# Performance work log

Hardware: AMD Instinct MI355X
Metric: run time of the kernel (lower is better)

Reference implementation:

```python
import jax, jax.numpy as jnp
import numpy as np

D_MODEL = 1024
NHEAD = 16
HEAD_DIM = D_MODEL // NHEAD


def setup_inputs() -> dict:
    key = jax.random.key(0)
    ks = jax.random.split(key, 7)
    N, S, E = 2, 2048, D_MODEL
    query = jax.random.normal(ks[0], (N, S, E), dtype=jnp.float32)
    key_t = jax.random.normal(ks[1], (N, S, E), dtype=jnp.float32)
    value = jax.random.normal(ks[2], (N, S, E), dtype=jnp.float32)
    # nn.Linear default init scale ~ 1/sqrt(fan_in)
    s = 1.0 / np.sqrt(E)
    w_in = jax.random.uniform(ks[3], (3 * E, E), jnp.float32, -s, s)
    b_in = jax.random.uniform(ks[4], (3 * E,), jnp.float32, -s, s)
    w_o = jax.random.uniform(ks[5], (E, E), jnp.float32, -s, s)
    b_o = jax.random.uniform(ks[6], (E,), jnp.float32, -s, s)
    return {"query": query, "key": key_t, "value": value,
            "w_in": w_in, "b_in": b_in, "w_o": w_o, "b_o": b_o}


def reference(query, key, value, w_in, b_in, w_o, b_o):
    # NOTE: the torch module computes q,k,v all from `query` (self-attention);
    # the `key`/`value` args are ignored by its forward math.
    N, S, E = query.shape
    H, Dh = NHEAD, HEAD_DIM
    qkv = query @ w_in.T + b_in                      # (N, S, 3E)
    q, k, v = jnp.split(qkv, 3, axis=-1)
    def heads(x):
        return x.reshape(N, S, H, Dh).transpose(0, 2, 1, 3)  # (N, H, S, Dh)
    q, k, v = heads(q), heads(k), heads(v)
    scale = 1.0 / jnp.sqrt(jnp.asarray(Dh, query.dtype))
    scores = jnp.einsum('bhqd,bhkd->bhqk', q, k) * scale     # (N, H, S, S)
    attn = jax.nn.softmax(scores, axis=-1)
    out = jnp.einsum('bhqk,bhkd->bhqd', attn, v)             # (N, H, S, Dh)
    out = out.transpose(0, 2, 1, 3).reshape(N, S, E)
    return out @ w_o.T + b_o
```

## Files before the change

### kernel.cpp

```cpp
#include <hip/hip_runtime.h>
#include <hip/hip_bf16.h>
#include <stdint.h>

#define NB   2
#define SEQ  2048
#define EMB  1024
#define NH   16
#define DH   64
#define MR   (NB*SEQ)
#define E3   (3*EMB)
#define CSC  (0.125f * 1.44269504f)

typedef __attribute__((ext_vector_type(8))) short bf16x8;
typedef __attribute__((ext_vector_type(4))) float f32x4;
typedef __attribute__((ext_vector_type(16))) float f32x16;

__device__ __forceinline__ unsigned short f2bf(float f) {
  unsigned u = __float_as_uint(f);
  unsigned r = (u + 0x7FFF + ((u >> 16) & 1)) >> 16;
  return (unsigned short)r;
}
__device__ __forceinline__ unsigned pack2(float lo, float hi) {
  return (unsigned)f2bf(lo) | ((unsigned)f2bf(hi) << 16);
}
__device__ __forceinline__ float bf2f(unsigned short s) {
  return __uint_as_float(((unsigned)s) << 16);
}
__device__ __forceinline__ unsigned cvtpk(float lo, float hi) {
  unsigned r;
  asm("v_cvt_pk_bf16_f32 %0, %1, %2" : "=v"(r) : "v"(lo), "v"(hi));
  return r;
}

__device__ __forceinline__ void gld16(const unsigned short* g, unsigned short* l) {
  __builtin_amdgcn_global_load_lds(
      (const __attribute__((address_space(1))) unsigned int*)g,
      (__attribute__((address_space(3))) unsigned int*)l,
      16, 0, 0);
}

__global__ void cvt_all(const float* __restrict__ q,
                        const float* __restrict__ w_in,
                        const float* __restrict__ w_o,
                        unsigned short* __restrict__ Xbf,
                        unsigned short* __restrict__ Winbf,
                        unsigned short* __restrict__ Wobf) {
  int b = blockIdx.x;
  const float* src; unsigned short* dst; int off;
  if (b < 2048)      { src = q;    dst = Xbf;   off = b; }
  else if (b < 3584) { src = w_in; dst = Winbf; off = b - 2048; }
  else               { src = w_o;  dst = Wobf;  off = b - 3584; }
  int i = (off * 256 + threadIdx.x) * 8;
  float4 a = *(const float4*)(src + i);
  float4 c = *(const float4*)(src + i + 4);
  uint4 o;
  o.x = pack2(a.x, a.y);
  o.y = pack2(a.z, a.w);
  o.z = pack2(c.x, c.y);
  o.w = pack2(c.z, c.w);
  *(uint4*)(dst + i) = o;
}

template<int BN, bool OUT_F32>
__global__ __launch_bounds__(256) void gemm_bt(
    const unsigned short* __restrict__ A,
    const unsigned short* __restrict__ Bt,
    const float* __restrict__ bias,
    void* __restrict__ Cout,
    int K, int ldc, int scale_cols) {
  constexpr int NR = BN / 32;
  constexpr int WNT = BN / 2;
  __shared__ unsigned short As[4096];
  __shared__ unsigned short Bs[BN * 32];
  const int tid  = threadIdx.x;
  const int lane = tid & 63;
  const int w    = tid >> 6;
  const int wm = w >> 1, wn = w & 1;
  const int g = lane >> 4, li = lane & 15;
  const int rowBase = blockIdx.x * 128;
  const int colBase = blockIdx.y * BN;

  f32x4 acc[4][NR];
#pragma unroll
  for (int m = 0; m < 4; ++m)
#pragma unroll
    for (int nn = 0; nn < NR; ++nn) { acc[m][nn][0]=0.f; acc[m][nn][1]=0.f; acc[m][nn][2]=0.f; acc[m][nn][3]=0.f; }

  const unsigned short* Ag = A  + (size_t)(rowBase + (tid >> 2)) * K + (tid & 3) * 8;
  const unsigned short* Bg = Bt + (size_t)(colBase + (tid >> 2)) * K + (tid & 3) * 8;

  for (int k0 = 0; k0 < K; k0 += 32) {
    __syncthreads();
    gld16(Ag + k0,                As + tid * 8);
    gld16(Ag + (size_t)64*K + k0, As + 2048 + tid * 8);
    gld16(Bg + k0,                Bs + tid * 8);
    if (BN == 128)
      gld16(Bg + (size_t)64*K + k0, Bs + 2048 + tid * 8);
    __syncthreads();

    bf16x8 af[4], bfv[NR];
#pragma unroll
    for (int m = 0; m < 4; ++m)
      af[m] = *(const bf16x8*)&As[(wm*64 + m*16 + li) * 32 + g * 8];
#pragma unroll
    for (int nn = 0; nn < NR; ++nn)
      bfv[nn] = *(const bf16x8*)&Bs[(wn*WNT + nn*16 + li) * 32 + g * 8];
#pragma unroll
    for (int m = 0; m < 4; ++m)
#pragma unroll
      for (int nn = 0; nn < NR; ++nn)
        acc[m][nn] = __builtin_amdgcn_mfma_f32_16x16x32_bf16(af[m], bfv[nn], acc[m][nn], 0, 0, 0);
  }

#pragma unroll
  for (int nn = 0; nn < NR; ++nn) {
    const int col = colBase + wn*WNT + nn*16 + li;
    const float bv = bias[col];
    const float sc = (col < scale_cols) ? CSC : 1.0f;
#pragma unroll
    for (int m = 0; m < 4; ++m) {
      const int r0 = rowBase + wm*64 + m*16 + g*4;
#pragma unroll
      for (int r = 0; r < 4; ++r) {
        float v = (acc[m][nn][r] + bv) * sc;
        if (OUT_F32) ((float*)Cout)[(size_t)(r0 + r) * ldc + col] = v;
        else ((unsigned short*)Cout)[(size_t)(r0 + r) * ldc + col] = f2bf(v);
      }
    }
  }
}

__global__ __launch_bounds__(256, 3) void attn32(
    const unsigned short* __restrict__ qkv,
    unsigned short* __restrict__ x2) {
  __shared__ unsigned short smem[16384];
  char* LB = (char*)smem;

  const int tid  = threadIdx.x;
  const int lane = tid & 63;
  const int w    = tid >> 6;
  const int hi   = lane >> 5;
  const int l31  = lane & 31;
  const int slot = blockIdx.x;
  const int bid  = (slot & 7) * 64 + (slot >> 3);
  const int qb = bid & 15, h = (bid >> 4) & 15, n = bid >> 8;
  const size_t rowN = (size_t)n * SEQ;
  const int vp_ = tid & 31, dblk = tid >> 5;
  const int vps = (vp_ & ~6) | ((vp_ & 2) << 1) | ((vp_ & 4) >> 1);

  bf16x8 qf[4];
  {
    const size_t qr = rowN + qb*128 + w*32 + l31;
#pragma unroll
    for (int kc = 0; kc < 4; ++kc)
      qf[kc] = *(const bf16x8*)&qkv[qr * E3 + h*64 + kc*16 + hi*8];
  }

  f32x16 ZEROV;
#pragma unroll
  for (int i = 0; i < 16; ++i) ZEROV[i] = 0.f;
  f32x16 acc0 = ZEROV, acc1 = ZEROV;
  float ssum[8];
#pragma unroll
  for (int i = 0; i < 8; ++i) ssum[i] = 0.f;

  uint4 pv0, pv1;
  auto stageK = [&](int kt, int buf) {
#pragma unroll
    for (int p = 0; p < 2; ++p) {
      int r = p*32 + (tid >> 3);
      int ch = (tid & 7) ^ (r & 7);
      gld16(&qkv[(rowN + kt + r) * E3 + EMB + h*64 + ch*8],
            &smem[buf*4096 + p*2048 + tid*8]);
    }
  };
  auto loadV = [&](int kt) {
    const unsigned short* vp = &qkv[(rowN + kt + 2*vp_) * E3 + 2*EMB + h*64 + dblk*8];
    pv0 = *(const uint4*)vp;
    pv1 = *(const uint4*)(vp + E3);
  };
  auto writeV = [&](int buf) {
    const unsigned short* s0 = (const unsigned short*)&pv0;
    const unsigned short* s1 = (const unsigned short*)&pv1;
#pragma unroll
    for (int j = 0; j < 8; ++j) {
      int d = dblk*8 + j;
      unsigned val = (unsigned)s0[j] | ((unsigned)s1[j] << 16);
      *(unsigned*)(LB + 16384 + buf*8192 + d*128 + (((vps>>2) ^ (d&7)) << 4) + (vps&3)*4) = val;
    }
  };

  loadV(0);
  stageK(0, 0);
  writeV(0);
  __syncthreads();

  for (int t = 0; t < 32; ++t) {
    const int cur = t & 1;
    const bool pre = (t + 1 < 32);
    const int ktn = (t + 1) * 64;
    if (pre) { loadV(ktn); stageK(ktn, cur^1); }

    const char* Kb = LB + cur*8192;
    bf16x8 ka[4], kb[4];
#pragma unroll
    for (int kc = 0; kc < 4; ++kc) {
      const int sw = ((kc*2 + hi) ^ (l31 & 7)) << 4;
      ka[kc] = *(const bf16x8*)(Kb + l31*128 + sw);
      kb[kc] = *(const bf16x8*)(Kb + 4096 + l31*128 + sw);
    }
    __builtin_amdgcn_s_setprio(1);
    f32x16 z0 = __builtin_amdgcn_mfma_f32_32x32x16_bf16(ka[0], qf[0], ZEROV, 0, 0, 0);
    f32x16 z1 = __builtin_amdgcn_mfma_f32_32x32x16_bf16(kb[0], qf[0], ZEROV, 0, 0, 0);
#pragma unroll
    for (int kc = 1; kc < 4; ++kc) {
      z0 = __builtin_amdgcn_mfma_f32_32x32x16_bf16(ka[kc], qf[kc], z0, 0, 0, 0);
      z1 = __builtin_amdgcn_mfma_f32_32x32x16_bf16(kb[kc], qf[kc], z1, 0, 0, 0);
    }
    __builtin_amdgcn_s_setprio(0);

#pragma unroll
    for (int i = 0; i < 16; ++i) {
      z0[i] = __builtin_amdgcn_exp2f(z0[i]);
      z1[i] = __builtin_amdgcn_exp2f(z1[i]);
    }
#pragma unroll
    for (int i = 0; i < 8; ++i)
      ssum[i] += (z0[2*i] + z0[2*i+1]) + (z1[2*i] + z1[2*i+1]);

    bf16x8 pf[4];
    {
      union { bf16x8 v; unsigned u[4]; } r0_, r1_, r2_, r3_;
#pragma unroll
      for (int j = 0; j < 4; ++j) {
        r0_.u[j] = cvtpk(z0[2*j],     z0[2*j + 1]);
        r1_.u[j] = cvtpk(z0[8 + 2*j], z0[9 + 2*j]);
        r2_.u[j] = cvtpk(z1[2*j],     z1[2*j + 1]);
        r3_.u[j] = cvtpk(z1[8 + 2*j], z1[9 + 2*j]);
      }
      pf[0] = r0_.v; pf[1] = r1_.v; pf[2] = r2_.v; pf[3] = r3_.v;
    }

    if (pre) writeV(cur ^ 1);

    const char* Vb = LB + 16384 + cur*8192;
    __builtin_amdgcn_s_setprio(1);
#pragma unroll
    for (int c = 0; c < 4; ++c) {
      const int sw = ((c*2 + hi) ^ (l31 & 7)) << 4;
      bf16x8 va = *(const bf16x8*)(Vb + l31*128 + sw);
      bf16x8 vb = *(const bf16x8*)(Vb + 4096 + l31*128 + sw);
      acc0 = __builtin_amdgcn_mfma_f32_32x32x16_bf16(va, pf[c], acc0, 0, 0, 0);
      acc1 = __builtin_amdgcn_mfma_f32_32x32x16_bf16(vb, pf[c], acc1, 0, 0, 0);
    }
    __builtin_amdgcn_s_setprio(0);
    __syncthreads();
  }

#pragma unroll
  for (int st = 4; st; st >>= 1)
#pragma unroll
    for (int i = 0; i < st; ++i) ssum[i] += ssum[i + st];
  float lsum = ssum[0] + __shfl_xor(ssum[0], 32);

  float rn = 1.0f / lsum;
  const int qrow_l = w*32 + l31;
#pragma unroll
  for (int dt = 0; dt < 2; ++dt) {
#pragma unroll
    for (int r = 0; r < 16; r += 2) {
      float v0 = (dt ? acc1[r]   : acc0[r])   * rn;
      float v1 = (dt ? acc1[r+1] : acc0[r+1]) * rn;
      int d = dt*32 + (r & 3) + 8*(r >> 2) + 4*hi;
      unsigned val = pack2(v0, v1);
      int col32 = d >> 1;
      int g = col32 >> 2;
      *(unsigned*)(LB + qrow_l*128 + ((g ^ (qrow_l & 7)) << 4) + (col32 & 3)*4) = val;
    }
  }
  __syncthreads();
  {
    int row = tid >> 1;
    size_t orow = (rowN + qb*128 + row) * EMB + h*64;
#pragma unroll
    for (int i = 0; i < 4; ++i) {
      int gg = (tid & 1)*4 + i;
      uint4 v = *(const uint4*)(LB + row*128 + ((gg ^ (row & 7)) << 4));
      *(uint4*)&x2[orow + gg*8] = v;
    }
  }
}

extern "C" void kernel_launch(void* const* d_in, const int* in_sizes, int n_in,
                              void* d_out, int out_size, void* d_ws, size_t ws_size,
                              hipStream_t stream) {
  const float* q    = (const float*)d_in[0];
  const float* w_in = (const float*)d_in[3];
  const float* b_in = (const float*)d_in[4];
  const float* w_o  = (const float*)d_in[5];
  const float* b_o  = (const float*)d_in[6];

  char* ws = (char*)d_ws;
  unsigned short* Wobf  = (unsigned short*)(ws);
  unsigned short* Xbf   = (unsigned short*)(ws + 2097152);
  unsigned short* Winbf = (unsigned short*)(ws + 10485760);
  unsigned short* QKV   = (unsigned short*)(ws + 16777216);
  unsigned short* X2    = (unsigned short*)(ws + 41943040);

  cvt_all<<<4096, 256, 0, stream>>>(q, w_in, w_o, Xbf, Winbf, Wobf);

  gemm_bt<128, false><<<dim3(32, 24), 256, 0, stream>>>(Xbf, Winbf, b_in, (void*)QKV, EMB, E3, 1024);
  attn32<<<NB * NH * (SEQ / 128), 256, 0, stream>>>(QKV, X2);
  gemm_bt<64, true><<<dim3(32, 16), 256, 0, stream>>>(X2, Wobf, b_o, d_out, EMB, EMB, 0);
}
```

Measured before the change: 117.0 us.

## Process two 64-key tiles per barrier in attention loop

Each main-loop iteration of the attention kernel now stages and consumes 128 keys (two 64-row K/V sub-tiles) instead of 64. That halves the number of __syncthreads barriers and prefetch rounds. Shared memory doubles to 64KB and launch bounds drop from 3 to 2 blocks per CU, trading occupancy for fewer synchronisations and larger prefetch batches. More V data is held in registers during prefetch, which raises register pressure.

Result: no change. 117.4 us (+0.3%).

```diff
diff --git a/kernel.cpp b/kernel.cpp
--- a/kernel.cpp
+++ b/kernel.cpp
@@ -130,10 +130,10 @@
   }
 }
 
-__global__ __launch_bounds__(256, 3) void attn32(
+__global__ __launch_bounds__(256, 2) void attn32(
     const unsigned short* __restrict__ qkv,
     unsigned short* __restrict__ x2) {
-  __shared__ unsigned short smem[16384];
+  __shared__ unsigned short smem[32768];
   char* LB = (char*)smem;
 
   const int tid  = threadIdx.x;
@@ -164,96 +164,111 @@
 #pragma unroll
   for (int i = 0; i < 8; ++i) ssum[i] = 0.f;
 
-  uint4 pv0, pv1;
-  auto stageK = [&](int kt, int buf) {
+  uint4 pvA0, pvA1, pvB0, pvB1;
+
+  auto stageK = [&](int kt, int base) {
 #pragma unroll
     for (int p = 0; p < 2; ++p) {
       int r = p*32 + (tid >> 3);
       int ch = (tid & 7) ^ (r & 7);
       gld16(&qkv[(rowN + kt + r) * E3 + EMB + h*64 + ch*8],
-            &smem[buf*4096 + p*2048 + tid*8]);
+            &smem[base + p*2048 + tid*8]);
     }
   };
-  auto loadV = [&](int kt) {
+  auto loadV = [&](int kt, uint4& v0, uint4& v1) {
     const unsigned short* vp = &qkv[(rowN + kt + 2*vp_) * E3 + 2*EMB + h*64 + dblk*8];
-    pv0 = *(const uint4*)vp;
-    pv1 = *(const uint4*)(vp + E3);
+    v0 = *(const uint4*)vp;
+    v1 = *(const uint4*)(vp + E3);
   };
-  auto writeV = [&](int buf) {
-    const unsigned short* s0 = (const unsigned short*)&pv0;
-    const unsigned short* s1 = (const unsigned short*)&pv1;
+  auto writeV = [&](int base, const uint4& v0, const uint4& v1) {
+    const unsigned short* s0 = (const unsigned short*)&v0;
+    const unsigned short* s1 = (const unsigned short*)&v1;
 #pragma unroll
     for (int j = 0; j < 8; ++j) {
       int d = dblk*8 + j;
       unsigned val = (unsigned)s0[j] | ((unsigned)s1[j] << 16);
-      *(unsigned*)(LB + 16384 + buf*8192 + d*128 + (((vps>>2) ^ (d&7)) << 4) + (vps&3)*4) = val;
+      *(unsigned*)(LB + base + d*128 + (((vps>>2) ^ (d&7)) << 4) + (vps&3)*4) = val;
     }
   };
 
-  loadV(0);
-  stageK(0, 0);
-  writeV(0);
+  loadV(0,  pvA0, pvA1);
+  loadV(64, pvB0, pvB1);
+  stageK(0,  0);
+  stageK(64, 4096);
+  writeV(32768,        pvA0, pvA1);
+  writeV(32768 + 8192, pvB0, pvB1);
   __syncthreads();
 
-  for (int t = 0; t < 32; ++t) {
+  for (int t = 0; t < 16; ++t) {
     const int cur = t & 1;
-    const bool pre = (t + 1 < 32);
-    const int ktn = (t + 1) * 64;
-    if (pre) { loadV(ktn); stageK(ktn, cur^1); }
-
-    const char* Kb = LB + cur*8192;
-    bf16x8 ka[4], kb[4];
-#pragma unroll
-    for (int kc = 0; kc < 4; ++kc) {
-      const int sw = ((kc*2 + hi) ^ (l31 & 7)) << 4;
-      ka[kc] = *(const bf16x8*)(Kb + l31*128 + sw);
-      kb[kc] = *(const bf16x8*)(Kb + 4096 + l31*128 + sw);
-    }
-    __builtin_amdgcn_s_setprio(1);
-    f32x16 z0 = __builtin_amdgcn_mfma_f32_32x32x16_bf16(ka[0], qf[0], ZEROV, 0, 0, 0);
-    f32x16 z1 = __builtin_amdgcn_mfma_f32_32x32x16_bf16(kb[0], qf[0], ZEROV, 0, 0, 0);
-#pragma unroll
-    for (int kc = 1; kc < 4; ++kc) {
-      z0 = __builtin_amdgcn_mfma_f32_32x32x16_bf16(ka[kc], qf[kc], z0, 0, 0, 0);
-      z1 = __builtin_amdgcn_mfma_f32_32x32x16_bf16(kb[kc], qf[kc], z1, 0, 0, 0);
-    }
-    __builtin_amdgcn_s_setprio(0);
-
-#pragma unroll
-    for (int i = 0; i < 16; ++i) {
-      z0[i] = __builtin_amdgcn_exp2f(z0[i]);
-      z1[i] = __builtin_amdgcn_exp2f(z1[i]);
-    }
-#pragma unroll
-    for (int i = 0; i < 8; ++i)
-      ssum[i] += (z0[2*i] + z0[2*i+1]) + (z1[2*i] + z1[2*i+1]);
-
-    bf16x8 pf[4];
-    {
-      union { bf16x8 v; unsigned u[4]; } r0_, r1_, r2_, r3_;
-#pragma unroll
-      for (int j = 0; j < 4; ++j) {
-        r0_.u[j] = cvtpk(z0[2*j],     z0[2*j + 1]);
-        r1_.u[j] = cvtpk(z0[8 + 2*j], z0[9 + 2*j]);
-        r2_.u[j] = cvtpk(z1[2*j],     z1[2*j + 1]);
-        r3_.u[j] = cvtpk(z1[8 + 2*j], z1[9 + 2*j]);
-      }
-      pf[0] = r0_.v; pf[1] = r1_.v; pf[2] = r2_.v; pf[3] = r3_.v;
-    }
-
-    if (pre) writeV(cur ^ 1);
-
-    const char* Vb = LB + 16384 + cur*8192;
-    __builtin_amdgcn_s_setprio(1);
-#pragma unroll
-    for (int c = 0; c < 4; ++c) {
-      const int sw = ((c*2 + hi) ^ (l31 & 7)) << 4;
-      bf16x8 va = *(const bf16x8*)(Vb + l31*128 + sw);
-      bf16x8 vb = *(const bf16x8*)(Vb + 4096 + l31*128 + sw);
-      acc0 = __builtin_amdgcn_mfma_f32_32x32x16_bf16(va, pf[c], acc0, 0, 0, 0);
-      acc1 = __builtin_amdgcn_mfma_f32_32x32x16_bf16(vb, pf[c], acc1, 0, 0, 0);
-    }
-    __builtin_amdgcn_s_setprio(0);
+    const bool pre = (t + 1 < 16);
+    const int ktn = (t + 1) * 128;
+    if (pre) {
+      loadV(ktn,      pvA0, pvA1);
+      loadV(ktn + 64, pvB0, pvB1);
+      stageK(ktn,      (cur^1)*8192);
+      stageK(ktn + 64, (cur^1)*8192 + 4096);
+    }
+
+#pragma unroll
+    for (int sub = 0; sub < 2; ++sub) {
+      const char* Kb = LB + (cur*2 + sub)*8192;
+      bf16x8 ka[4], kb[4];
+#pragma unroll
+      for (int kc = 0; kc < 4; ++kc) {
+        const int sw = ((kc*2 + hi) ^ (l31 & 7)) << 4;
+        ka[kc] = *(const bf16x8*)(Kb + l31*128 + sw);
+        kb[kc] = *(const bf16x8*)(Kb + 4096 + l31*128 + sw);
+      }
+      __builtin_amdgcn_s_setprio(1);
+      f32x16 z0 = __builtin_amdgcn_mfma_f32_32x32x16_bf16(ka[0], qf[0], ZEROV, 0, 0, 0);
+      f32x16 z1 = __builtin_amdgcn_mfma_f32_32x32x16_bf16(kb[0], qf[0], ZEROV, 0, 0, 0);
+#pragma unroll
+      for (int kc = 1; kc < 4; ++kc) {
+        z0 = __builtin_amdgcn_mfma_f32_32x32x16_bf16(ka[kc], qf[kc], z0, 0, 0, 0);
+        z1 = __builtin_amdgcn_mfma_f32_32x32x16_bf16(kb[kc], qf[kc], z1, 0, 0, 0);
+      }
+      __builtin_amdgcn_s_setprio(0);
+
+#pragma unroll
+      for (int i = 0; i < 16; ++i) {
+        z0[i] = __builtin_amdgcn_exp2f(z0[i]);
+        z1[i] = __builtin_amdgcn_exp2f(z1[i]);
+      }
+#pragma unroll
+      for (int i = 0; i < 8; ++i)
+        ssum[i] += (z0[2*i] + z0[2*i+1]) + (z1[2*i] + z1[2*i+1]);
+
+      bf16x8 pf[4];
+      {
+        union { bf16x8 v; unsigned u[4]; } r0_, r1_, r2_, r3_;
+#pragma unroll
+        for (int j = 0; j < 4; ++j) {
+          r0_.u[j] = cvtpk(z0[2*j],     z0[2*j + 1]);
+          r1_.u[j] = cvtpk(z0[8 + 2*j], z0[9 + 2*j]);
+          r2_.u[j] = cvtpk(z1[2*j],     z1[2*j + 1]);
+          r3_.u[j] = cvtpk(z1[8 + 2*j], z1[9 + 2*j]);
+        }
+        pf[0] = r0_.v; pf[1] = r1_.v; pf[2] = r2_.v; pf[3] = r3_.v;
+      }
+
+      if (sub == 0 && pre) {
+        writeV(32768 + (cur^1)*16384,        pvA0, pvA1);
+        writeV(32768 + (cur^1)*16384 + 8192, pvB0, pvB1);
+      }
+
+      const char* Vb = LB + 32768 + (cur*2 + sub)*8192;
+      __builtin_amdgcn_s_setprio(1);
+#pragma unroll
+      for (int c = 0; c < 4; ++c) {
+        const int sw = ((c*2 + hi) ^ (l31 & 7)) << 4;
+        bf16x8 va = *(const bf16x8*)(Vb + l31*128 + sw);
+        bf16x8 vb = *(const bf16x8*)(Vb + 4096 + l31*128 + sw);
+        acc0 = __builtin_amdgcn_mfma_f32_32x32x16_bf16(va, pf[c], acc0, 0, 0, 0);
+        acc1 = __builtin_amdgcn_mfma_f32_32x32x16_bf16(vb, pf[c], acc1, 0, 0, 0);
+      }
+      __builtin_amdgcn_s_setprio(0);
+    }
     __syncthreads();
   }
 
```

## Process two query subtiles per wave to reuse K/V tiles in attention

Applied to the files above, without the earlier changes.

Each attention block now covers 256 query rows, with every wave computing two 32-row query groups against the same K and V LDS tiles. The aim is to halve K/V global loads and LDS staging per query and to amortise the barriers. In exchange the grid halves to one block per CU, register pressure rises (launch bounds lowered to 1), and there are fewer waves to hide latency.

Result: slower. 124.6 us (+6.5%).

```diff
diff --git a/kernel.cpp b/kernel.cpp
--- a/kernel.cpp
+++ b/kernel.cpp
@@ -130,7 +130,7 @@
   }
 }
 
-__global__ __launch_bounds__(256, 3) void attn32(
+__global__ __launch_bounds__(256, 1) void attn32(
     const unsigned short* __restrict__ qkv,
     unsigned short* __restrict__ x2) {
   __shared__ unsigned short smem[16384];
@@ -142,27 +142,30 @@
   const int hi   = lane >> 5;
   const int l31  = lane & 31;
   const int slot = blockIdx.x;
-  const int bid  = (slot & 7) * 64 + (slot >> 3);
-  const int qb = bid & 15, h = (bid >> 4) & 15, n = bid >> 8;
+  const int bid  = (slot & 7) * 32 + (slot >> 3);
+  const int qb = bid & 7, h = (bid >> 3) & 15, n = bid >> 7;
   const size_t rowN = (size_t)n * SEQ;
   const int vp_ = tid & 31, dblk = tid >> 5;
   const int vps = (vp_ & ~6) | ((vp_ & 2) << 1) | ((vp_ & 4) >> 1);
 
-  bf16x8 qf[4];
+  bf16x8 qf[2][4];
   {
-    const size_t qr = rowN + qb*128 + w*32 + l31;
-#pragma unroll
-    for (int kc = 0; kc < 4; ++kc)
-      qf[kc] = *(const bf16x8*)&qkv[qr * E3 + h*64 + kc*16 + hi*8];
+    const size_t qr0 = rowN + qb*256 + w*64 + l31;
+#pragma unroll
+    for (int g = 0; g < 2; ++g)
+#pragma unroll
+      for (int kc = 0; kc < 4; ++kc)
+        qf[g][kc] = *(const bf16x8*)&qkv[(qr0 + g*32) * E3 + h*64 + kc*16 + hi*8];
   }
 
   f32x16 ZEROV;
 #pragma unroll
   for (int i = 0; i < 16; ++i) ZEROV[i] = 0.f;
-  f32x16 acc0 = ZEROV, acc1 = ZEROV;
-  float ssum[8];
-#pragma unroll
-  for (int i = 0; i < 8; ++i) ssum[i] = 0.f;
+  f32x16 aA0 = ZEROV, aA1 = ZEROV;
+  f32x16 aB0 = ZEROV, aB1 = ZEROV;
+  float sA[8], sB[8];
+#pragma unroll
+  for (int i = 0; i < 8; ++i) { sA[i] = 0.f; sB[i] = 0.f; }
 
   uint4 pv0, pv1;
   auto stageK = [&](int kt, int buf) {
@@ -209,16 +212,16 @@
       ka[kc] = *(const bf16x8*)(Kb + l31*128 + sw);
       kb[kc] = *(const bf16x8*)(Kb + 4096 + l31*128 + sw);
     }
+
     __builtin_amdgcn_s_setprio(1);
-    f32x16 z0 = __builtin_amdgcn_mfma_f32_32x32x16_bf16(ka[0], qf[0], ZEROV, 0, 0, 0);
-    f32x16 z1 = __builtin_amdgcn_mfma_f32_32x32x16_bf16(kb[0], qf[0], ZEROV, 0, 0, 0);
+    f32x16 z0 = __builtin_amdgcn_mfma_f32_32x32x16_bf16(ka[0], qf[0][0], ZEROV, 0, 0, 0);
+    f32x16 z1 = __builtin_amdgcn_mfma_f32_32x32x16_bf16(kb[0], qf[0][0], ZEROV, 0, 0, 0);
 #pragma unroll
     for (int kc = 1; kc < 4; ++kc) {
-      z0 = __builtin_amdgcn_mfma_f32_32x32x16_bf16(ka[kc], qf[kc], z0, 0, 0, 0);
-      z1 = __builtin_amdgcn_mfma_f32_32x32x16_bf16(kb[kc], qf[kc], z1, 0, 0, 0);
+      z0 = __builtin_amdgcn_mfma_f32_32x32x16_bf16(ka[kc], qf[0][kc], z0, 0, 0, 0);
+      z1 = __builtin_amdgcn_mfma_f32_32x32x16_bf16(kb[kc], qf[0][kc], z1, 0, 0, 0);
     }
     __builtin_amdgcn_s_setprio(0);
-
 #pragma unroll
     for (int i = 0; i < 16; ++i) {
       z0[i] = __builtin_amdgcn_exp2f(z0[i]);
@@ -226,9 +229,8 @@
     }
 #pragma unroll
     for (int i = 0; i < 8; ++i)
-      ssum[i] += (z0[2*i] + z0[2*i+1]) + (z1[2*i] + z1[2*i+1]);
-
-    bf16x8 pf[4];
+      sA[i] += (z0[2*i] + z0[2*i+1]) + (z1[2*i] + z1[2*i+1]);
+    bf16x8 pf0[4];
     {
       union { bf16x8 v; unsigned u[4]; } r0_, r1_, r2_, r3_;
 #pragma unroll
@@ -238,20 +240,61 @@
         r2_.u[j] = cvtpk(z1[2*j],     z1[2*j + 1]);
         r3_.u[j] = cvtpk(z1[8 + 2*j], z1[9 + 2*j]);
       }
-      pf[0] = r0_.v; pf[1] = r1_.v; pf[2] = r2_.v; pf[3] = r3_.v;
+      pf0[0] = r0_.v; pf0[1] = r1_.v; pf0[2] = r2_.v; pf0[3] = r3_.v;
     }
 
     if (pre) writeV(cur ^ 1);
 
     const char* Vb = LB + 16384 + cur*8192;
-    __builtin_amdgcn_s_setprio(1);
+    bf16x8 va[4], vb[4];
 #pragma unroll
     for (int c = 0; c < 4; ++c) {
       const int sw = ((c*2 + hi) ^ (l31 & 7)) << 4;
-      bf16x8 va = *(const bf16x8*)(Vb + l31*128 + sw);
-      bf16x8 vb = *(const bf16x8*)(Vb + 4096 + l31*128 + sw);
-      acc0 = __builtin_amdgcn_mfma_f32_32x32x16_bf16(va, pf[c], acc0, 0, 0, 0);
-      acc1 = __builtin_amdgcn_mfma_f32_32x32x16_bf16(vb, pf[c], acc1, 0, 0, 0);
+      va[c] = *(const bf16x8*)(Vb + l31*128 + sw);
+      vb[c] = *(const bf16x8*)(Vb + 4096 + l31*128 + sw);
+    }
+    __builtin_amdgcn_s_setprio(1);
+#pragma unroll
+    for (int c = 0; c < 4; ++c) {
+      aA0 = __builtin_amdgcn_mfma_f32_32x32x16_bf16(va[c], pf0[c], aA0, 0, 0, 0);
+      aA1 = __builtin_amdgcn_mfma_f32_32x32x16_bf16(vb[c], pf0[c], aA1, 0, 0, 0);
+    }
+    __builtin_amdgcn_s_setprio(0);
+
+    __builtin_amdgcn_s_setprio(1);
+    f32x16 y0 = __builtin_amdgcn_mfma_f32_32x32x16_bf16(ka[0], qf[1][0], ZEROV, 0, 0, 0);
+    f32x16 y1 = __builtin_amdgcn_mfma_f32_32x32x16_bf16(kb[0], qf[1][0], ZEROV, 0, 0, 0);
+#pragma unroll
+    for (int kc = 1; kc < 4; ++kc) {
+      y0 = __builtin_amdgcn_mfma_f32_32x32x16_bf16(ka[kc], qf[1][kc], y0, 0, 0, 0);
+      y1 = __builtin_amdgcn_mfma_f32_32x32x16_bf16(kb[kc], qf[1][kc], y1, 0, 0, 0);
+    }
+    __builtin_amdgcn_s_setprio(0);
+#pragma unroll
+    for (int i = 0; i < 16; ++i) {
+      y0[i] = __builtin_amdgcn_exp2f(y0[i]);
+      y1[i] = __builtin_amdgcn_exp2f(y1[i]);
+    }
+#pragma unroll
+    for (int i = 0; i < 8; ++i)
+      sB[i] += (y0[2*i] + y0[2*i+1]) + (y1[2*i] + y1[2*i+1]);
+    bf16x8 pf1[4];
+    {
+      union { bf16x8 v; unsigned u[4]; } r0_, r1_, r2_, r3_;
+#pragma unroll
+      for (int j = 0; j < 4; ++j) {
+        r0_.u[j] = cvtpk(y0[2*j],     y0[2*j + 1]);
+        r1_.u[j] = cvtpk(y0[8 + 2*j], y0[9 + 2*j]);
+        r2_.u[j] = cvtpk(y1[2*j],     y1[2*j + 1]);
+        r3_.u[j] = cvtpk(y1[8 + 2*j], y1[9 + 2*j]);
+      }
+      pf1[0] = r0_.v; pf1[1] = r1_.v; pf1[2] = r2_.v; pf1[3] = r3_.v;
+    }
+    __builtin_amdgcn_s_setprio(1);
+#pragma unroll
+    for (int c = 0; c < 4; ++c) {
+      aB0 = __builtin_amdgcn_mfma_f32_32x32x16_bf16(va[c], pf1[c], aB0, 0, 0, 0);
+      aB1 = __builtin_amdgcn_mfma_f32_32x32x16_bf16(vb[c], pf1[c], aB1, 0, 0, 0);
     }
     __builtin_amdgcn_s_setprio(0);
     __syncthreads();
@@ -260,28 +303,38 @@
 #pragma unroll
   for (int st = 4; st; st >>= 1)
 #pragma unroll
-    for (int i = 0; i < st; ++i) ssum[i] += ssum[i + st];
-  float lsum = ssum[0] + __shfl_xor(ssum[0], 32);
-
-  float rn = 1.0f / lsum;
-  const int qrow_l = w*32 + l31;
+    for (int i = 0; i < st; ++i) { sA[i] += sA[i + st]; sB[i] += sB[i + st]; }
+  float lsumA = sA[0] + __shfl_xor(sA[0], 32);
+  float lsumB = sB[0] + __shfl_xor(sB[0], 32);
+  float rnA = 1.0f / lsumA;
+  float rnB = 1.0f / lsumB;
+
+  const int qrA = w*64 + l31;
+  const int qrB = w*64 + 32 + l31;
 #pragma unroll
   for (int dt = 0; dt < 2; ++dt) {
 #pragma unroll
     for (int r = 0; r < 16; r += 2) {
-      float v0 = (dt ? acc1[r]   : acc0[r])   * rn;
-      float v1 = (dt ? acc1[r+1] : acc0[r+1]) * rn;
       int d = dt*32 + (r & 3) + 8*(r >> 2) + 4*hi;
-      unsigned val = pack2(v0, v1);
       int col32 = d >> 1;
       int g = col32 >> 2;
-      *(unsigned*)(LB + qrow_l*128 + ((g ^ (qrow_l & 7)) << 4) + (col32 & 3)*4) = val;
+      {
+        float v0 = (dt ? aA1[r]   : aA0[r])   * rnA;
+        float v1 = (dt ? aA1[r+1] : aA0[r+1]) * rnA;
+        *(unsigned*)(LB + qrA*128 + ((g ^ (qrA & 7)) << 4) + (col32 & 3)*4) = pack2(v0, v1);
+      }
+      {
+        float v0 = (dt ? aB1[r]   : aB0[r])   * rnB;
+        float v1 = (dt ? aB1[r+1] : aB0[r+1]) * rnB;
+        *(unsigned*)(LB + qrB*128 + ((g ^ (qrB & 7)) << 4) + (col32 & 3)*4) = pack2(v0, v1);
+      }
     }
   }
   __syncthreads();
-  {
-    int row = tid >> 1;
-    size_t orow = (rowN + qb*128 + row) * EMB + h*64;
+#pragma unroll
+  for (int p = 0; p < 2; ++p) {
+    int row = p*128 + (tid >> 1);
+    size_t orow = (rowN + qb*256 + row) * EMB + h*64;
 #pragma unroll
     for (int i = 0; i < 4; ++i) {
       int gg = (tid & 1)*4 + i;
@@ -310,6 +363,6 @@
   cvt_all<<<4096, 256, 0, stream>>>(q, w_in, w_o, Xbf, Winbf, Wobf);
 
   gemm_bt<128, false><<<dim3(32, 24), 256, 0, stream>>>(Xbf, Winbf, b_in, (void*)QKV, EMB, E3, 1024);
-  attn32<<<NB * NH * (SEQ / 128), 256, 0, stream>>>(QKV, X2);
+  attn32<<<NB * NH * (SEQ / 256), 256, 0, stream>>>(QKV, X2);
   gemm_bt<64, true><<<dim3(32, 16), 256, 0, stream>>>(X2, Wobf, b_o, d_out, EMB, EMB, 0);
 }
```

## Software-pipeline QK^T of next tile with softmax/PV of previous tile

Applied to the files above, without the earlier changes.

Restructures the attention loop so the QK^T MFMAs for tile t+1 are issued alongside the exp/softmax and PV work for tile t, using two sets of score registers. The V buffer becomes a 4-deep ring, which grows LDS from 32KB to 48KB. Launch bounds drop from 3 to 2 blocks per CU. The aim is to overlap exp (VALU) with MFMA and hide latency, at the cost of more registers, more LDS and lower occupancy.

After: 115.9 us. No clear change (-0.9%).

```diff
diff --git a/kernel.cpp b/kernel.cpp
--- a/kernel.cpp
+++ b/kernel.cpp
@@ -130,10 +130,10 @@
   }
 }
 
-__global__ __launch_bounds__(256, 3) void attn32(
+__global__ __launch_bounds__(256, 2) void attn32(
     const unsigned short* __restrict__ qkv,
     unsigned short* __restrict__ x2) {
-  __shared__ unsigned short smem[16384];
+  __shared__ unsigned short smem[24576];
   char* LB = (char*)smem;
 
   const int tid  = threadIdx.x;
@@ -179,28 +179,17 @@
     pv0 = *(const uint4*)vp;
     pv1 = *(const uint4*)(vp + E3);
   };
-  auto writeV = [&](int buf) {
+  auto writeV = [&](int vb) {
     const unsigned short* s0 = (const unsigned short*)&pv0;
     const unsigned short* s1 = (const unsigned short*)&pv1;
 #pragma unroll
     for (int j = 0; j < 8; ++j) {
       int d = dblk*8 + j;
       unsigned val = (unsigned)s0[j] | ((unsigned)s1[j] << 16);
-      *(unsigned*)(LB + 16384 + buf*8192 + d*128 + (((vps>>2) ^ (d&7)) << 4) + (vps&3)*4) = val;
-    }
-  };
-
-  loadV(0);
-  stageK(0, 0);
-  writeV(0);
-  __syncthreads();
-
-  for (int t = 0; t < 32; ++t) {
-    const int cur = t & 1;
-    const bool pre = (t + 1 < 32);
-    const int ktn = (t + 1) * 64;
-    if (pre) { loadV(ktn); stageK(ktn, cur^1); }
-
+      *(unsigned*)(LB + 16384 + vb*8192 + d*128 + (((vps>>2) ^ (d&7)) << 4) + (vps&3)*4) = val;
+    }
+  };
+  auto QK = [&](int cur, f32x16& o0, f32x16& o1) {
     const char* Kb = LB + cur*8192;
     bf16x8 ka[4], kb[4];
 #pragma unroll
@@ -210,15 +199,16 @@
       kb[kc] = *(const bf16x8*)(Kb + 4096 + l31*128 + sw);
     }
     __builtin_amdgcn_s_setprio(1);
-    f32x16 z0 = __builtin_amdgcn_mfma_f32_32x32x16_bf16(ka[0], qf[0], ZEROV, 0, 0, 0);
-    f32x16 z1 = __builtin_amdgcn_mfma_f32_32x32x16_bf16(kb[0], qf[0], ZEROV, 0, 0, 0);
+    o0 = __builtin_amdgcn_mfma_f32_32x32x16_bf16(ka[0], qf[0], ZEROV, 0, 0, 0);
+    o1 = __builtin_amdgcn_mfma_f32_32x32x16_bf16(kb[0], qf[0], ZEROV, 0, 0, 0);
 #pragma unroll
     for (int kc = 1; kc < 4; ++kc) {
-      z0 = __builtin_amdgcn_mfma_f32_32x32x16_bf16(ka[kc], qf[kc], z0, 0, 0, 0);
-      z1 = __builtin_amdgcn_mfma_f32_32x32x16_bf16(kb[kc], qf[kc], z1, 0, 0, 0);
+      o0 = __builtin_amdgcn_mfma_f32_32x32x16_bf16(ka[kc], qf[kc], o0, 0, 0, 0);
+      o1 = __builtin_amdgcn_mfma_f32_32x32x16_bf16(kb[kc], qf[kc], o1, 0, 0, 0);
     }
     __builtin_amdgcn_s_setprio(0);
-
+  };
+  auto SMPV = [&](int vb, f32x16& z0, f32x16& z1) {
 #pragma unroll
     for (int i = 0; i < 16; ++i) {
       z0[i] = __builtin_amdgcn_exp2f(z0[i]);
@@ -227,7 +217,6 @@
 #pragma unroll
     for (int i = 0; i < 8; ++i)
       ssum[i] += (z0[2*i] + z0[2*i+1]) + (z1[2*i] + z1[2*i+1]);
-
     bf16x8 pf[4];
     {
       union { bf16x8 v; unsigned u[4]; } r0_, r1_, r2_, r3_;
@@ -240,22 +229,45 @@
       }
       pf[0] = r0_.v; pf[1] = r1_.v; pf[2] = r2_.v; pf[3] = r3_.v;
     }
-
-    if (pre) writeV(cur ^ 1);
-
-    const char* Vb = LB + 16384 + cur*8192;
+    const char* Vb = LB + 16384 + vb*8192;
     __builtin_amdgcn_s_setprio(1);
 #pragma unroll
     for (int c = 0; c < 4; ++c) {
       const int sw = ((c*2 + hi) ^ (l31 & 7)) << 4;
       bf16x8 va = *(const bf16x8*)(Vb + l31*128 + sw);
-      bf16x8 vb = *(const bf16x8*)(Vb + 4096 + l31*128 + sw);
-      acc0 = __builtin_amdgcn_mfma_f32_32x32x16_bf16(va, pf[c], acc0, 0, 0, 0);
-      acc1 = __builtin_amdgcn_mfma_f32_32x32x16_bf16(vb, pf[c], acc1, 0, 0, 0);
+      bf16x8 vb_ = *(const bf16x8*)(Vb + 4096 + l31*128 + sw);
+      acc0 = __builtin_amdgcn_mfma_f32_32x32x16_bf16(va,  pf[c], acc0, 0, 0, 0);
+      acc1 = __builtin_amdgcn_mfma_f32_32x32x16_bf16(vb_, pf[c], acc1, 0, 0, 0);
     }
     __builtin_amdgcn_s_setprio(0);
+  };
+
+  f32x16 zA0, zA1, zB0, zB1;
+
+  loadV(0); stageK(0, 0); writeV(0);
+  __syncthreads();
+  loadV(64); stageK(64, 1);
+  QK(0, zA0, zA1);
+  writeV(1);
+  __syncthreads();
+
+  for (int t = 1; t + 1 < 32; t += 2) {
+    loadV((t + 1) * 64); stageK((t + 1) * 64, (t + 1) & 1);
+    QK(t & 1, zB0, zB1);
+    SMPV((t - 1) & 3, zA0, zA1);
+    writeV((t + 1) & 3);
     __syncthreads();
-  }
+    const bool pre = (t + 2 < 32);
+    if (pre) { loadV((t + 2) * 64); stageK((t + 2) * 64, (t + 2) & 1); }
+    QK((t + 1) & 1, zA0, zA1);
+    SMPV(t & 3, zB0, zB1);
+    if (pre) writeV((t + 2) & 3);
+    __syncthreads();
+  }
+
+  QK(1, zB0, zB1);
+  SMPV(30 & 3, zA0, zA1);
+  SMPV(31 & 3, zB0, zB1);
 
 #pragma unroll
   for (int st = 4; st; st >>= 1)
@@ -263,6 +275,7 @@
     for (int i = 0; i < st; ++i) ssum[i] += ssum[i + st];
   float lsum = ssum[0] + __shfl_xor(ssum[0], 32);
 
+  __syncthreads();
   float rn = 1.0f / lsum;
   const int qrow_l = w*32 + l31;
 #pragma unroll
```
